# Performance work log

Measured on AMD Instinct MI355X. Metric: run time of the kernel, lower is better.

Reference implementation:

```python
import jax, jax.numpy as jnp
import numpy as np

N = 50000      # nodes (single coalesced node type)
IN = 256       # in_dim
H = 8          # attention heads
D = 64         # hidden_dim (per-head out dim)
HD = H * D     # 512, fused feature dim
OUT = 64       # final out_dim
M = 2          # meta-paths
E = 800000     # edges per meta-path graph
SEM_HID = 128  # SemanticAttention hidden size (DGL/OpenHGNN default)
NEG_SLOPE = 0.2


def setup_inputs() -> dict:
    key = jax.random.key(0)
    ks = jax.random.split(key, 13)
    s = 0.05
    return {
        "x": jax.random.normal(ks[0], (N, IN), jnp.float32),
        "src": jax.random.randint(ks[1], (M, E), 0, N, jnp.int32),
        "dst": jax.random.randint(ks[2], (M, E), 0, N, jnp.int32),
        # per-metapath GATConv params
        "Wg": jax.random.normal(ks[3], (M, IN, HD), jnp.float32) * s,
        "al": jax.random.normal(ks[4], (M, H, D), jnp.float32) * s,
        "ar": jax.random.normal(ks[5], (M, H, D), jnp.float32) * s,
        "bg": jax.random.normal(ks[6], (M, HD), jnp.float32) * s,
        # semantic attention: Linear(HD,128) -> tanh -> Linear(128,1,no bias)
        "W1": jax.random.normal(ks[7], (HD, SEM_HID), jnp.float32) * s,
        "b1": jax.random.normal(ks[8], (SEM_HID,), jnp.float32) * s,
        "q": jax.random.normal(ks[9], (SEM_HID,), jnp.float32) * s,
        # final linear
        "Wout": jax.random.normal(ks[10], (HD, OUT), jnp.float32) * s,
        "bout": jax.random.normal(ks[11], (OUT,), jnp.float32) * s,
    }


def _gat(x, W, al, ar, b, src, dst):
    # x: [N, IN] -> feat: [N, H, D]
    feat = (x @ W).reshape(N, H, D)
    el = jnp.sum(feat * al, axis=-1)                      # [N, H]
    er = jnp.sum(feat * ar, axis=-1)                      # [N, H]
    e = jax.nn.leaky_relu(el[src] + er[dst], NEG_SLOPE)   # [E, H]
    # edge softmax per destination node (allow zero in-degree)
    m = jax.ops.segment_max(e, dst, num_segments=N)       # [N, H]
    m = jnp.where(jnp.isfinite(m), m, 0.0)
    ex = jnp.exp(e - m[dst])                              # [E, H]
    den = jax.ops.segment_sum(ex, dst, num_segments=N)    # [N, H]
    alpha = ex / jnp.maximum(den[dst], 1e-9)              # [E, H]
    # scatter-aggregate messages: [E, H, D] -> [N, H, D]
    out = jax.ops.segment_sum(alpha[:, :, None] * feat[src], dst, num_segments=N)
    return jax.nn.elu(out.reshape(N, HD) + b)             # flatten heads + bias + elu


def reference(x, src, dst, Wg, al, ar, bg, W1, b1, q, Wout, bout):
    # per-metapath GAT (loop over M=2 structurally distinct graphs)
    zs = [_gat(x, Wg[p], al[p], ar[p], bg[p], src[p], dst[p]) for p in range(M)]
    z = jnp.stack(zs, axis=1)                             # [N, M, HD]
    # semantic attention fusion
    w = jnp.mean(jnp.tanh(z @ W1 + b1) @ q, axis=0)       # [M]
    beta = jax.nn.softmax(w)                              # [M]
    fused = jnp.einsum("nmf,m->nf", z, beta)             # [N, HD]
    # final linear
    return fused @ Wout + bout                            # [N, OUT]
```

## Files before the change

kernel.cpp:

```cpp
#include <hip/hip_runtime.h>
#include <cstdint>

#define N_NODES 50000
#define IN_DIM 256
#define H_HEADS 8
#define D_HEAD 64
#define HD 512
#define OUT_DIM 64
#define M_PATHS 2
#define E_EDGES 800000
#define SEM_HID 128
#define NEG_SLOPE 0.2f
#define ELL_CAP 64

typedef __attribute__((ext_vector_type(8))) short bf16x8;
typedef __attribute__((ext_vector_type(4))) float f32x4;
typedef __attribute__((ext_vector_type(8))) unsigned short u16x8;

__device__ __forceinline__ float b2f(unsigned short u) {
  return __uint_as_float(((unsigned)u) << 16);
}
__device__ __forceinline__ unsigned short f2b(float f) {
  unsigned u = __float_as_uint(f);
  unsigned r = (u + 0x7fffu + ((u >> 16) & 1u)) >> 16;
  return (unsigned short)r;
}

__device__ __forceinline__ float eluf(float x) {
  return x > 0.f ? x : (expf(x) - 1.f);
}
__device__ __forceinline__ float lrelu(float x) {
  return x > 0.f ? x : NEG_SLOPE * x;
}

__global__ void k_prep(const float* __restrict__ Wg, const float* __restrict__ W1,
                       const float* __restrict__ Wout, unsigned short* __restrict__ WgbT,
                       unsigned short* __restrict__ W1T, unsigned short* __restrict__ WoutT) {
  int gid = blockIdx.x * blockDim.x + threadIdx.x;
  if (gid < 262144) {
    int m = gid >> 17, r = gid & 131071, n = r >> 8, k = r & 255;
    WgbT[(size_t)m * 131072 + n * 256 + k] = f2b(Wg[(size_t)m * 131072 + k * 512 + n]);
  } else if (gid < 327680) {
    int r = gid - 262144; int c = r >> 9, k = r & 511;
    W1T[c * 512 + k] = f2b(W1[k * 128 + c]);
  } else if (gid < 360448) {
    int r = gid - 327680; int c = r >> 9, k = r & 511;
    WoutT[c * 512 + k] = f2b(Wout[k * 64 + c]);
  }
}

__global__ void k_edge_e(const int* __restrict__ src, const int* __restrict__ dst,
                         int* __restrict__ deg, int* __restrict__ ell_src) {
  int e = blockIdx.x * blockDim.x + threadIdx.x;
  if (e >= E_EDGES) return;
  int d = dst[e];
  int p = atomicAdd(&deg[d], 1);
  if (p < ELL_CAP) ell_src[d * ELL_CAP + p] = src[e];
}

__global__ __launch_bounds__(256) void k_gemm_feat(const float* __restrict__ xfp,
                                                   const unsigned short* __restrict__ BT,
                                                   const float* __restrict__ al,
                                                   const float* __restrict__ ar,
                                                   unsigned short* __restrict__ C,
                                                   float* __restrict__ el,
                                                   float* __restrict__ er) {
  __shared__ __align__(16) unsigned short As[64][72];
  __shared__ __align__(16) unsigned short Bs[256][72];
  const int tid = threadIdx.x;
  const int r0 = blockIdx.x * 64, c0 = blockIdx.y * 256;
  const int w = tid >> 6, lane = tid & 63;
  const int cl = lane & 15, kg = lane >> 4;
  const int rw = (w >> 1) * 32;
  const int cw = (w & 1) * 128;
  f32x4 acc[2][8] = {};
  for (int k0 = 0; k0 < IN_DIM; k0 += 64) {
#pragma unroll
    for (int p = 0; p < 2; ++p) {
      int idx = tid + p * 256;
      int row = idx >> 3, ko = (idx & 7) * 8;
      u16x8 v = (u16x8)(unsigned short)0;
      int grow = r0 + row;
      if (grow < N_NODES) {
        const float4* g = (const float4*)&xfp[(size_t)grow * IN_DIM + k0 + ko];
        float4 g0 = g[0], g1 = g[1];
        v[0] = f2b(g0.x); v[1] = f2b(g0.y); v[2] = f2b(g0.z); v[3] = f2b(g0.w);
        v[4] = f2b(g1.x); v[5] = f2b(g1.y); v[6] = f2b(g1.z); v[7] = f2b(g1.w);
      }
      *(u16x8*)&As[row][ko] = v;
    }
#pragma unroll
    for (int p = 0; p < 8; ++p) {
      int idx = tid + p * 256;
      int col = idx >> 3, ko = (idx & 7) * 8;
      *(u16x8*)&Bs[col][ko] = *(const u16x8*)&BT[(size_t)(c0 + col) * IN_DIM + k0 + ko];
    }
    __syncthreads();
#pragma unroll
    for (int kk = 0; kk < 64; kk += 32) {
      bf16x8 a0 = *(const bf16x8*)&As[rw + cl][kk + kg * 8];
      bf16x8 a1 = *(const bf16x8*)&As[rw + 16 + cl][kk + kg * 8];
#pragma unroll
      for (int ct = 0; ct < 8; ++ct) {
        bf16x8 b = *(const bf16x8*)&Bs[cw + ct * 16 + cl][kk + kg * 8];
        acc[0][ct] = __builtin_amdgcn_mfma_f32_16x16x32_bf16(a0, b, acc[0][ct], 0, 0, 0);
        acc[1][ct] = __builtin_amdgcn_mfma_f32_16x16x32_bf16(a1, b, acc[1][ct], 0, 0, 0);
      }
    }
    __syncthreads();
  }
  const int ccol = c0 + cw;
#pragma unroll
  for (int rt = 0; rt < 2; ++rt)
#pragma unroll
    for (int ct = 0; ct < 8; ++ct)
#pragma unroll
      for (int reg = 0; reg < 4; ++reg) {
        int row = r0 + rw + rt * 16 + kg * 4 + reg;
        if (row < N_NODES) C[(size_t)row * HD + ccol + ct * 16 + cl] = f2b(acc[rt][ct][reg]);
      }
  const int hb = ccol >> 6;
#pragma unroll
  for (int g = 0; g < 2; ++g) {
    float elp[2][4] = {};
    float erp[2][4] = {};
#pragma unroll
    for (int cc = 0; cc < 4; ++cc) {
      int ct = g * 4 + cc;
      float av = al[(hb + g) * 64 + cc * 16 + cl];
      float rv = ar[(hb + g) * 64 + cc * 16 + cl];
#pragma unroll
      for (int rt = 0; rt < 2; ++rt)
#pragma unroll
        for (int reg = 0; reg < 4; ++reg) {
          elp[rt][reg] += acc[rt][ct][reg] * av;
          erp[rt][reg] += acc[rt][ct][reg] * rv;
        }
    }
#pragma unroll
    for (int off = 1; off < 16; off <<= 1)
#pragma unroll
      for (int rt = 0; rt < 2; ++rt)
#pragma unroll
        for (int reg = 0; reg < 4; ++reg) {
          elp[rt][reg] += __shfl_xor(elp[rt][reg], off);
          erp[rt][reg] += __shfl_xor(erp[rt][reg], off);
        }
    if (cl == 0) {
#pragma unroll
      for (int rt = 0; rt < 2; ++rt)
#pragma unroll
        for (int reg = 0; reg < 4; ++reg) {
          int row = r0 + rw + rt * 16 + kg * 4 + reg;
          if (row < N_NODES) {
            el[row * 8 + hb + g] = elp[rt][reg];
            er[row * 8 + hb + g] = erp[rt][reg];
          }
        }
    }
  }
}

__global__ __launch_bounds__(256) void k_agg(const unsigned short* __restrict__ featb,
                                             const float* __restrict__ el,
                                             const float* __restrict__ er,
                                             const int* __restrict__ ell_src,
                                             const int* __restrict__ deg,
                                             const float* __restrict__ bg,
                                             unsigned short* __restrict__ z) {
  __shared__ float lds_ex[4][544];
  const int tid = threadIdx.x;
  const int widx = tid >> 6, lane = tid & 63;
  const int n = blockIdx.x * 4 + widx;
  const int h = lane >> 3;
  const int dcnt = min(deg[n], ELL_CAP);
  float evf[8];
#pragma unroll
  for (int j = 0; j < 8; ++j) evf[j] = -1e30f;
  int s_reg = 0;
  if (lane < dcnt) {
    s_reg = ell_src[n * ELL_CAP + lane];
    const float4* e4 = (const float4*)&el[s_reg * 8];
    float4 a0 = e4[0], a1 = e4[1];
    const float4* r4 = (const float4*)&er[n * 8];
    float4 b0 = r4[0], b1v = r4[1];
    evf[0] = lrelu(a0.x + b0.x); evf[1] = lrelu(a0.y + b0.y);
    evf[2] = lrelu(a0.z + b0.z); evf[3] = lrelu(a0.w + b0.w);
    evf[4] = lrelu(a1.x + b1v.x); evf[5] = lrelu(a1.y + b1v.y);
    evf[6] = lrelu(a1.z + b1v.z); evf[7] = lrelu(a1.w + b1v.w);
  }
  float mx[8];
#pragma unroll
  for (int j = 0; j < 8; ++j) mx[j] = evf[j];
#pragma unroll
  for (int off = 1; off < 64; off <<= 1)
#pragma unroll
    for (int j = 0; j < 8; ++j) mx[j] = fmaxf(mx[j], __shfl_xor(mx[j], off));
#pragma unroll
  for (int j = 0; j < 8; ++j) {
    float exv = (lane < dcnt) ? expf(evf[j] - mx[j]) : 0.f;
    lds_ex[widx][j * 68 + lane] = exv;
  }
  float acc[8] = {};
  float densum = 0.f;
  const float* exrow = &lds_ex[widx][h * 68];
  const unsigned short* fb = featb + lane * 8;
  int i = 0;
  for (; i + 4 <= dcnt; i += 4) {
    int s0 = __shfl(s_reg, i),     s1 = __shfl(s_reg, i + 1);
    int s2 = __shfl(s_reg, i + 2), s3 = __shfl(s_reg, i + 3);
    float w0 = exrow[i], w1 = exrow[i + 1], w2 = exrow[i + 2], w3 = exrow[i + 3];
    u16x8 f0 = *(const u16x8*)&fb[(size_t)s0 * HD];
    u16x8 f1 = *(const u16x8*)&fb[(size_t)s1 * HD];
    u16x8 f2 = *(const u16x8*)&fb[(size_t)s2 * HD];
    u16x8 f3 = *(const u16x8*)&fb[(size_t)s3 * HD];
    densum += (w0 + w1) + (w2 + w3);
#pragma unroll
    for (int j = 0; j < 8; ++j) acc[j] += w0 * b2f(f0[j]);
#pragma unroll
    for (int j = 0; j < 8; ++j) acc[j] += w1 * b2f(f1[j]);
#pragma unroll
    for (int j = 0; j < 8; ++j) acc[j] += w2 * b2f(f2[j]);
#pragma unroll
    for (int j = 0; j < 8; ++j) acc[j] += w3 * b2f(f3[j]);
  }
  for (; i < dcnt; ++i) {
    int s0 = __shfl(s_reg, i);
    float w0 = exrow[i];
    u16x8 f0 = *(const u16x8*)&fb[(size_t)s0 * HD];
    densum += w0;
#pragma unroll
    for (int j = 0; j < 8; ++j) acc[j] += w0 * b2f(f0[j]);
  }
  float ds = 1.f / fmaxf(densum, 1e-9f);
  const float4* bg4 = (const float4*)&bg[lane * 8];
  float4 bga = bg4[0], bgb = bg4[1];
  float bgv[8] = {bga.x, bga.y, bga.z, bga.w, bgb.x, bgb.y, bgb.z, bgb.w};
  u16x8 zo;
#pragma unroll
  for (int j = 0; j < 8; ++j) zo[j] = f2b(eluf(acc[j] * ds + bgv[j]));
  *(u16x8*)&z[(size_t)n * HD + lane * 8] = zo;
}

__global__ __launch_bounds__(256) void k_gemm_post(const unsigned short* __restrict__ Zb,
                                                   const unsigned short* __restrict__ W1T,
                                                   const unsigned short* __restrict__ WoutT,
                                                   const float* __restrict__ b1,
                                                   const float* __restrict__ qv,
                                                   float* __restrict__ wsem_m,
                                                   unsigned short* __restrict__ yb) {
  __shared__ __align__(16) unsigned short As[64][72];
  __shared__ __align__(16) unsigned short Bs[192][72];
  __shared__ float redv[16];
  const int tid = threadIdx.x;
  const int r0 = blockIdx.x * 64;
  const int w = tid >> 6, lane = tid & 63;
  const int cl = lane & 15, kg = lane >> 4;
  f32x4 acc[12] = {};
  for (int k0 = 0; k0 < HD; k0 += 64) {
#pragma unroll
    for (int p = 0; p < 2; ++p) {
      int idx = tid + p * 256;
      int row = idx >> 3, ko = (idx & 7) * 8;
      u16x8 v = (u16x8)(unsigned short)0;
      if (r0 + row < N_NODES) v = *(const u16x8*)&Zb[(size_t)(r0 + row) * HD + k0 + ko];
      *(u16x8*)&As[row][ko] = v;
    }
#pragma unroll
    for (int p = 0; p < 6; ++p) {
      int idx = tid + p * 256;
      int col = idx >> 3, ko = (idx & 7) * 8;
      u16x8 v = (col < 128) ? *(const u16x8*)&W1T[(size_t)col * HD + k0 + ko]
                            : *(const u16x8*)&WoutT[(size_t)(col - 128) * HD + k0 + ko];
      *(u16x8*)&Bs[col][ko] = v;
    }
    __syncthreads();
#pragma unroll
    for (int kk = 0; kk < 64; kk += 32) {
      bf16x8 a = *(const bf16x8*)&As[w * 16 + cl][kk + kg * 8];
#pragma unroll
      for (int ct = 0; ct < 12; ++ct) {
        bf16x8 b = *(const bf16x8*)&Bs[ct * 16 + cl][kk + kg * 8];
        acc[ct] = __builtin_amdgcn_mfma_f32_16x16x32_bf16(a, b, acc[ct], 0, 0, 0);
      }
    }
    __syncthreads();
  }
  float rs[4] = {0.f, 0.f, 0.f, 0.f};
#pragma unroll
  for (int ct = 0; ct < 8; ++ct) {
    int col = ct * 16 + cl;
    float bb = b1[col], qq = qv[col];
#pragma unroll
    for (int reg = 0; reg < 4; ++reg) rs[reg] += tanhf(acc[ct][reg] + bb) * qq;
  }
#pragma unroll
  for (int off = 1; off < 16; off <<= 1)
#pragma unroll
    for (int reg = 0; reg < 4; ++reg) rs[reg] += __shfl_xor(rs[reg], off);
  float val = 0.f;
#pragma unroll
  for (int reg = 0; reg < 4; ++reg) {
    int row = r0 + w * 16 + kg * 4 + reg;
    if (row < N_NODES) val += rs[reg];
  }
  if (cl == 0) redv[w * 4 + kg] = val;
  __syncthreads();
  if (tid == 0) {
    float sv = 0.f;
#pragma unroll
    for (int k = 0; k < 16; ++k) sv += redv[k];
    atomicAdd(wsem_m, sv);
  }
#pragma unroll
  for (int ct = 8; ct < 12; ++ct)
#pragma unroll
    for (int reg = 0; reg < 4; ++reg) {
      int row = r0 + w * 16 + kg * 4 + reg;
      if (row < N_NODES) yb[(size_t)row * OUT_DIM + (ct - 8) * 16 + cl] = f2b(acc[ct][reg]);
    }
}

__global__ void k_beta(const float* __restrict__ wsem, float* __restrict__ beta) {
  float w0 = wsem[0] / (float)N_NODES, w1 = wsem[1] / (float)N_NODES;
  float mx = fmaxf(w0, w1);
  float e0 = expf(w0 - mx), e1 = expf(w1 - mx);
  float inv = 1.f / (e0 + e1);
  beta[0] = e0 * inv;
  beta[1] = e1 * inv;
}

__global__ void k_final(const unsigned short* __restrict__ yb, const float* __restrict__ beta,
                        const float* __restrict__ bout, float* __restrict__ out) {
  int gid = blockIdx.x * blockDim.x + threadIdx.x;
  size_t off = (size_t)gid * 8;
  if (off >= (size_t)N_NODES * OUT_DIM) return;
  u16x8 ya = *(const u16x8*)&yb[off];
  u16x8 yc = *(const u16x8*)&yb[(size_t)N_NODES * OUT_DIM + off];
  float b0 = beta[0], b1v = beta[1];
  const int cb = (int)(off & 63);
#pragma unroll
  for (int j = 0; j < 8; ++j)
    out[off + j] = b0 * b2f(ya[j]) + b1v * b2f(yc[j]) + bout[cb + j];
}

extern "C" void kernel_launch(void* const* d_in, const int* in_sizes, int n_in,
                              void* d_out, int out_size, void* d_ws, size_t ws_size,
                              hipStream_t stream) {
  const float* x    = (const float*)d_in[0];
  const int*   src  = (const int*)d_in[1];
  const int*   dst  = (const int*)d_in[2];
  const float* Wg   = (const float*)d_in[3];
  const float* al   = (const float*)d_in[4];
  const float* ar   = (const float*)d_in[5];
  const float* bg   = (const float*)d_in[6];
  const float* W1   = (const float*)d_in[7];
  const float* b1   = (const float*)d_in[8];
  const float* q    = (const float*)d_in[9];
  const float* Wout = (const float*)d_in[10];
  const float* bout = (const float*)d_in[11];
  float* out = (float*)d_out;

  char* ws = (char*)d_ws;
  unsigned short* featb = (unsigned short*)(ws);
  unsigned short* z     = (unsigned short*)(ws + 51200000);
  unsigned short* yb    = (unsigned short*)(ws + 102400000);
  int* ell_src          = (int*)(ws + 115200000);
  float* el             = (float*)(ws + 128000000);
  float* er             = (float*)(ws + 129600000);
  int* deg              = (int*)(ws + 131200000);
  unsigned short* WgbT  = (unsigned short*)(ws + 131400064);
  unsigned short* W1T   = (unsigned short*)(ws + 131924352);
  unsigned short* WoutT = (unsigned short*)(ws + 132055424);
  float* wsem           = (float*)(ws + 132120960);
  float* beta           = (float*)(ws + 132121024);

  hipMemsetAsync(wsem, 0, 2 * sizeof(float), stream);
  k_prep<<<1408, 256, 0, stream>>>(Wg, W1, Wout, WgbT, W1T, WoutT);

  for (int m = 0; m < M_PATHS; ++m) {
    const int* srcm = src + (size_t)m * E_EDGES;
    const int* dstm = dst + (size_t)m * E_EDGES;
    hipMemsetAsync(deg, 0, N_NODES * sizeof(int), stream);
    k_edge_e<<<3125, 256, 0, stream>>>(srcm, dstm, deg, ell_src);
    dim3 gf(782, 2);
    k_gemm_feat<<<gf, 256, 0, stream>>>(x, WgbT + (size_t)m * 131072,
                                        al + m * HD, ar + m * HD, featb, el, er);
    k_agg<<<12500, 256, 0, stream>>>(featb, el, er, ell_src, deg, bg + m * HD, z);
    k_gemm_post<<<782, 256, 0, stream>>>(z, W1T, WoutT, b1, q, wsem + m,
                                         yb + (size_t)m * N_NODES * OUT_DIM);
  }
  k_beta<<<1, 1, 0, stream>>>(wsem, beta);
  k_final<<<1563, 256, 0, stream>>>(yb, beta, bout, out);
}
```

Measured before the change: 562.4 us.

## Prefetch edge loads unconditionally, unroll gather by 8, and double rows per post-GEMM block

In the aggregation kernel, the ELL source index, degree, er and el loads are now issued unconditionally, with the source index clamped into range. This removes the dependency on deg before the gathers start. The feature gather loop is unrolled to 8 outstanding row loads per iteration, giving more memory-level parallelism for the random gathers. The post GEMM now processes 128 rows per block with two MFMA row tiles per wave, so each B tile loaded into LDS is reused twice and the grid is halved. The cost is more VGPR pressure and possibly lower occupancy, and ELL slots beyond a node's degree are read even though their values are masked.

After: 580.8 us. 3.3% more time.

```diff
diff --git a/kernel.cpp b/kernel.cpp
--- a/kernel.cpp
+++ b/kernel.cpp
@@ -173,21 +173,23 @@
   const int widx = tid >> 6, lane = tid & 63;
   const int n = blockIdx.x * 4 + widx;
   const int h = lane >> 3;
-  const int dcnt = min(deg[n], ELL_CAP);
+  int s_raw = ell_src[n * ELL_CAP + lane];
+  int dcnt_raw = deg[n];
+  const float4* r4 = (const float4*)&er[n * 8];
+  float4 b0 = r4[0], b1v = r4[1];
+  int s_reg = ((unsigned)s_raw < (unsigned)N_NODES) ? s_raw : 0;
+  const float4* e4 = (const float4*)&el[s_reg * 8];
+  float4 a0 = e4[0], a1 = e4[1];
+  const int dcnt = min(dcnt_raw, ELL_CAP);
+  const bool valid = lane < dcnt;
   float evf[8];
-#pragma unroll
-  for (int j = 0; j < 8; ++j) evf[j] = -1e30f;
-  int s_reg = 0;
-  if (lane < dcnt) {
-    s_reg = ell_src[n * ELL_CAP + lane];
-    const float4* e4 = (const float4*)&el[s_reg * 8];
-    float4 a0 = e4[0], a1 = e4[1];
-    const float4* r4 = (const float4*)&er[n * 8];
-    float4 b0 = r4[0], b1v = r4[1];
-    evf[0] = lrelu(a0.x + b0.x); evf[1] = lrelu(a0.y + b0.y);
-    evf[2] = lrelu(a0.z + b0.z); evf[3] = lrelu(a0.w + b0.w);
-    evf[4] = lrelu(a1.x + b1v.x); evf[5] = lrelu(a1.y + b1v.y);
-    evf[6] = lrelu(a1.z + b1v.z); evf[7] = lrelu(a1.w + b1v.w);
+  evf[0] = lrelu(a0.x + b0.x); evf[1] = lrelu(a0.y + b0.y);
+  evf[2] = lrelu(a0.z + b0.z); evf[3] = lrelu(a0.w + b0.w);
+  evf[4] = lrelu(a1.x + b1v.x); evf[5] = lrelu(a1.y + b1v.y);
+  evf[6] = lrelu(a1.z + b1v.z); evf[7] = lrelu(a1.w + b1v.w);
+  if (!valid) {
+#pragma unroll
+    for (int j = 0; j < 8; ++j) evf[j] = -1e30f;
   }
   float mx[8];
 #pragma unroll
@@ -198,7 +200,7 @@
     for (int j = 0; j < 8; ++j) mx[j] = fmaxf(mx[j], __shfl_xor(mx[j], off));
 #pragma unroll
   for (int j = 0; j < 8; ++j) {
-    float exv = (lane < dcnt) ? expf(evf[j] - mx[j]) : 0.f;
+    float exv = valid ? expf(evf[j] - mx[j]) : 0.f;
     lds_ex[widx][j * 68 + lane] = exv;
   }
   float acc[8] = {};
@@ -206,23 +208,41 @@
   const float* exrow = &lds_ex[widx][h * 68];
   const unsigned short* fb = featb + lane * 8;
   int i = 0;
+  for (; i + 8 <= dcnt; i += 8) {
+    int ss[8];
+    float ww[8];
+    u16x8 ff[8];
+#pragma unroll
+    for (int u = 0; u < 8; ++u) {
+      ss[u] = __shfl(s_reg, i + u);
+      ww[u] = exrow[i + u];
+    }
+#pragma unroll
+    for (int u = 0; u < 8; ++u) ff[u] = *(const u16x8*)&fb[(size_t)ss[u] * HD];
+#pragma unroll
+    for (int u = 0; u < 8; ++u) {
+      densum += ww[u];
+#pragma unroll
+      for (int j = 0; j < 8; ++j) acc[j] += ww[u] * b2f(ff[u][j]);
+    }
+  }
   for (; i + 4 <= dcnt; i += 4) {
-    int s0 = __shfl(s_reg, i),     s1 = __shfl(s_reg, i + 1);
-    int s2 = __shfl(s_reg, i + 2), s3 = __shfl(s_reg, i + 3);
-    float w0 = exrow[i], w1 = exrow[i + 1], w2 = exrow[i + 2], w3 = exrow[i + 3];
-    u16x8 f0 = *(const u16x8*)&fb[(size_t)s0 * HD];
-    u16x8 f1 = *(const u16x8*)&fb[(size_t)s1 * HD];
-    u16x8 f2 = *(const u16x8*)&fb[(size_t)s2 * HD];
-    u16x8 f3 = *(const u16x8*)&fb[(size_t)s3 * HD];
-    densum += (w0 + w1) + (w2 + w3);
-#pragma unroll
-    for (int j = 0; j < 8; ++j) acc[j] += w0 * b2f(f0[j]);
-#pragma unroll
-    for (int j = 0; j < 8; ++j) acc[j] += w1 * b2f(f1[j]);
-#pragma unroll
-    for (int j = 0; j < 8; ++j) acc[j] += w2 * b2f(f2[j]);
-#pragma unroll
-    for (int j = 0; j < 8; ++j) acc[j] += w3 * b2f(f3[j]);
+    int ss[4];
+    float ww[4];
+    u16x8 ff[4];
+#pragma unroll
+    for (int u = 0; u < 4; ++u) {
+      ss[u] = __shfl(s_reg, i + u);
+      ww[u] = exrow[i + u];
+    }
+#pragma unroll
+    for (int u = 0; u < 4; ++u) ff[u] = *(const u16x8*)&fb[(size_t)ss[u] * HD];
+#pragma unroll
+    for (int u = 0; u < 4; ++u) {
+      densum += ww[u];
+#pragma unroll
+      for (int j = 0; j < 8; ++j) acc[j] += ww[u] * b2f(ff[u][j]);
+    }
   }
   for (; i < dcnt; ++i) {
     int s0 = __shfl(s_reg, i);
@@ -249,17 +269,18 @@
                                                    const float* __restrict__ qv,
                                                    float* __restrict__ wsem_m,
                                                    unsigned short* __restrict__ yb) {
-  __shared__ __align__(16) unsigned short As[64][72];
+  __shared__ __align__(16) unsigned short As[128][72];
   __shared__ __align__(16) unsigned short Bs[192][72];
   __shared__ float redv[16];
   const int tid = threadIdx.x;
-  const int r0 = blockIdx.x * 64;
+  const int r0 = blockIdx.x * 128;
   const int w = tid >> 6, lane = tid & 63;
   const int cl = lane & 15, kg = lane >> 4;
-  f32x4 acc[12] = {};
+  const int rw = w * 32;
+  f32x4 acc[2][12] = {};
   for (int k0 = 0; k0 < HD; k0 += 64) {
 #pragma unroll
-    for (int p = 0; p < 2; ++p) {
+    for (int p = 0; p < 4; ++p) {
       int idx = tid + p * 256;
       int row = idx >> 3, ko = (idx & 7) * 8;
       u16x8 v = (u16x8)(unsigned short)0;
@@ -277,33 +298,42 @@
     __syncthreads();
 #pragma unroll
     for (int kk = 0; kk < 64; kk += 32) {
-      bf16x8 a = *(const bf16x8*)&As[w * 16 + cl][kk + kg * 8];
+      bf16x8 a0 = *(const bf16x8*)&As[rw + cl][kk + kg * 8];
+      bf16x8 a1 = *(const bf16x8*)&As[rw + 16 + cl][kk + kg * 8];
 #pragma unroll
       for (int ct = 0; ct < 12; ++ct) {
         bf16x8 b = *(const bf16x8*)&Bs[ct * 16 + cl][kk + kg * 8];
-        acc[ct] = __builtin_amdgcn_mfma_f32_16x16x32_bf16(a, b, acc[ct], 0, 0, 0);
+        acc[0][ct] = __builtin_amdgcn_mfma_f32_16x16x32_bf16(a0, b, acc[0][ct], 0, 0, 0);
+        acc[1][ct] = __builtin_amdgcn_mfma_f32_16x16x32_bf16(a1, b, acc[1][ct], 0, 0, 0);
       }
     }
     __syncthreads();
   }
-  float rs[4] = {0.f, 0.f, 0.f, 0.f};
+  float rs[2][4] = {};
 #pragma unroll
   for (int ct = 0; ct < 8; ++ct) {
     int col = ct * 16 + cl;
     float bb = b1[col], qq = qv[col];
 #pragma unroll
-    for (int reg = 0; reg < 4; ++reg) rs[reg] += tanhf(acc[ct][reg] + bb) * qq;
+    for (int rt = 0; rt < 2; ++rt)
+#pragma unroll
+      for (int reg = 0; reg < 4; ++reg)
+        rs[rt][reg] += tanhf(acc[rt][ct][reg] + bb) * qq;
   }
 #pragma unroll
   for (int off = 1; off < 16; off <<= 1)
 #pragma unroll
-    for (int reg = 0; reg < 4; ++reg) rs[reg] += __shfl_xor(rs[reg], off);
+    for (int rt = 0; rt < 2; ++rt)
+#pragma unroll
+      for (int reg = 0; reg < 4; ++reg) rs[rt][reg] += __shfl_xor(rs[rt][reg], off);
   float val = 0.f;
 #pragma unroll
-  for (int reg = 0; reg < 4; ++reg) {
-    int row = r0 + w * 16 + kg * 4 + reg;
-    if (row < N_NODES) val += rs[reg];
-  }
+  for (int rt = 0; rt < 2; ++rt)
+#pragma unroll
+    for (int reg = 0; reg < 4; ++reg) {
+      int row = r0 + rw + rt * 16 + kg * 4 + reg;
+      if (row < N_NODES) val += rs[rt][reg];
+    }
   if (cl == 0) redv[w * 4 + kg] = val;
   __syncthreads();
   if (tid == 0) {
@@ -313,12 +343,15 @@
     atomicAdd(wsem_m, sv);
   }
 #pragma unroll
-  for (int ct = 8; ct < 12; ++ct)
-#pragma unroll
-    for (int reg = 0; reg < 4; ++reg) {
-      int row = r0 + w * 16 + kg * 4 + reg;
-      if (row < N_NODES) yb[(size_t)row * OUT_DIM + (ct - 8) * 16 + cl] = f2b(acc[ct][reg]);
-    }
+  for (int rt = 0; rt < 2; ++rt)
+#pragma unroll
+    for (int ct = 8; ct < 12; ++ct)
+#pragma unroll
+      for (int reg = 0; reg < 4; ++reg) {
+        int row = r0 + rw + rt * 16 + kg * 4 + reg;
+        if (row < N_NODES)
+          yb[(size_t)row * OUT_DIM + (ct - 8) * 16 + cl] = f2b(acc[rt][ct][reg]);
+      }
 }
 
 __global__ void k_beta(const float* __restrict__ wsem, float* __restrict__ beta) {
@@ -387,7 +420,7 @@
     k_gemm_feat<<<gf, 256, 0, stream>>>(x, WgbT + (size_t)m * 131072,
                                         al + m * HD, ar + m * HD, featb, el, er);
     k_agg<<<12500, 256, 0, stream>>>(featb, el, er, ell_src, deg, bg + m * HD, z);
-    k_gemm_post<<<782, 256, 0, stream>>>(z, W1T, WoutT, b1, q, wsem + m,
+    k_gemm_post<<<391, 256, 0, stream>>>(z, W1T, WoutT, b1, q, wsem + m,
                                          yb + (size_t)m * N_NODES * OUT_DIM);
   }
   k_beta<<<1, 1, 0, stream>>>(wsem, beta);
```
